# Kernel tuning notes

Measured on AMD Instinct MI355X. Metric: run time of the kernel, lower is better.

Reference implementation:

```python
import jax, jax.numpy as jnp
import numpy as np

N_NODES = 100000
IN_CH = 128
HID = 128
OUT_CH = 40
K = 3
N_EDGES = 3200000


def setup_inputs() -> dict:
    key = jax.random.key(0)
    ks = jax.random.split(key, 10)
    x = jax.random.normal(ks[0], (N_NODES, IN_CH), dtype=jnp.float32)
    edge_index = jax.random.randint(ks[1], (2, N_EDGES), 0, N_NODES, dtype=jnp.int64)
    s1 = 1.0 / np.sqrt(IN_CH)
    lin1_w = jax.random.uniform(ks[2], (IN_CH, HID), minval=-s1, maxval=s1, dtype=jnp.float32)
    lin1_b = jax.random.uniform(ks[3], (HID,), minval=-s1, maxval=s1, dtype=jnp.float32)
    s2 = 1.0 / np.sqrt(HID)
    gcn_w = jax.random.uniform(ks[4], (K, HID, HID), minval=-s2, maxval=s2, dtype=jnp.float32)
    gcn_b = jnp.zeros((K, HID), dtype=jnp.float32)
    lin2_w = jax.random.uniform(ks[5], (HID, OUT_CH), minval=-s2, maxval=s2, dtype=jnp.float32)
    lin2_b = jax.random.uniform(ks[6], (OUT_CH,), minval=-s2, maxval=s2, dtype=jnp.float32)
    return {"x": x, "edge_index": edge_index, "lin1_w": lin1_w, "lin1_b": lin1_b,
            "gcn_w": gcn_w, "gcn_b": gcn_b, "lin2_w": lin2_w, "lin2_b": lin2_b}


def _gcn_conv(h, w, b, src, dst, norm, n):
    # PyG GCNConv: transform, then symmetric-normalized aggregation (self-loops
    # already included in src/dst/norm), then bias.
    h = h @ w  # [N, H]
    msg = h[src] * norm[:, None]  # [E+N, H] gathered edge messages
    out = jax.ops.segment_sum(msg, dst, num_segments=n)
    return out + b


def reference(x, edge_index, lin1_w, lin1_b, gcn_w, gcn_b, lin2_w, lin2_b):
    n = x.shape[0]
    src, dst = edge_index[0], edge_index[1]
    # add self-loops (GCNConv default add_self_loops=True)
    loop = jnp.arange(n, dtype=src.dtype)
    src = jnp.concatenate([src, loop])
    dst = jnp.concatenate([dst, loop])
    # symmetric normalization D^{-1/2} (A+I) D^{-1/2}
    deg = jax.ops.segment_sum(jnp.ones(src.shape[0], dtype=x.dtype), dst, num_segments=n)
    dinv = jnp.where(deg > 0, jax.lax.rsqrt(deg), 0.0)
    norm = dinv[src] * dinv[dst]  # [E+N]

    h = jax.nn.relu(x @ lin1_w + lin1_b)  # dropout: eval mode (identity)
    for k in range(K):
        h = jax.nn.relu(_gcn_conv(h, gcn_w[k], gcn_b[k], src, dst, norm, n))
    logits = h @ lin2_w + lin2_b
    return jax.nn.log_softmax(logits, axis=1)
```

## Files before the change

kernel.cpp:

```cpp
#include <hip/hip_runtime.h>
#include <math.h>

#define NN 100000
#define NP 100032
#define HIDC 128
#define OUTC 40
#define NBUCK ((NN + 511) >> 9)
#define PT_TILE 8192
#define BCAP 18368
#define NRG 8
#define RG_SHIFT 14

typedef __attribute__((ext_vector_type(2))) float floatx2;
typedef __attribute__((ext_vector_type(4))) float floatx4;
typedef __attribute__((ext_vector_type(8))) short short8;
typedef __attribute__((ext_vector_type(4))) unsigned uintx4;

__device__ __forceinline__ unsigned pack_bf16x2(float a, float b) {
  unsigned ua = __float_as_uint(a), ub = __float_as_uint(b);
  ua = ua + 0x7fff + ((ua >> 16) & 1);
  ub = ub + 0x7fff + ((ub >> 16) & 1);
  return (ua >> 16) | (ub & 0xffff0000u);
}
__device__ __forceinline__ unsigned short bf16r(float x) {
  unsigned u = __float_as_uint(x);
  u = u + 0x7fff + ((u >> 16) & 1);
  return (unsigned short)(u >> 16);
}


__global__ __launch_bounds__(512) void partition_kernel(
    const int* __restrict__ src, const int* __restrict__ dst,
    int* __restrict__ bcur, unsigned* __restrict__ pairs, int E) {
  __shared__ int hist[256];
  __shared__ int lcur[256];
  __shared__ int startl[256];
  __shared__ int gofs[256];
  __shared__ unsigned lbuf[PT_TILE];
  int t = threadIdx.x;
  if (t < 256) { hist[t] = 0; lcur[t] = 0; }
  __syncthreads();
  int e0 = blockIdx.x * PT_TILE;
  int ec = E - e0; if (ec > PT_TILE) ec = PT_TILE;

  int dr[16], sr[16];
#pragma unroll
  for (int k = 0; k < 16; k++) {
    int i = t + (k << 9);
    if (i < ec) {
      int d = dst[e0 + i];
      dr[k] = d; sr[k] = src[e0 + i];
      atomicAdd(&hist[d >> 9], 1);
    }
  }
  __syncthreads();

  int h = (t < 256) ? hist[t] : 0;
  if (t < 256) startl[t] = h;
  __syncthreads();
  for (int off = 1; off < 256; off <<= 1) {
    int u = (t < 256 && t >= off) ? startl[t - off] : 0;
    __syncthreads();
    if (t < 256) startl[t] += u;
    __syncthreads();
  }
  if (t < 256) {
    int st = startl[t] - h;
    int gb = (h > 0) ? atomicAdd(&bcur[t], h) : 0;
    gofs[t] = gb - st;
    startl[t] = st;
  }
  __syncthreads();

#pragma unroll
  for (int k = 0; k < 16; k++) {
    int i = t + (k << 9);
    if (i < ec) {
      int d = dr[k];
      int b = d >> 9;
      int q = atomicAdd(&lcur[b], 1);
      lbuf[startl[b] + q] = ((unsigned)(d & 511) << 17) | (unsigned)sr[k];
    }
  }
  __syncthreads();

  for (int pos = t; pos < ec; pos += 512) {
    int lo = 0, hi = 255;
    while (lo < hi) {
      int mid = (lo + hi + 1) >> 1;
      if (startl[mid] <= pos) lo = mid; else hi = mid - 1;
    }
    pairs[gofs[lo] + pos] = lbuf[pos];
  }
}

__global__ __launch_bounds__(1024) void bucket_fill_kernel(
    const unsigned* __restrict__ pairs, const int* __restrict__ bcur,
    float* __restrict__ dinv, int* __restrict__ csr,
    int* __restrict__ sbeg, int* __restrict__ send,
    float* __restrict__ sdinv, int* __restrict__ sdn, int N) {
  int b = blockIdx.x;
  int d0 = b << 9;
  int nd = N - d0; if (nd > 512) nd = 512;
  __shared__ unsigned lbuf[BCAP];
  __shared__ unsigned short perm[BCAP];
  __shared__ int hist8[512 * NRG];
  __shared__ int cur8[512 * NRG];
  __shared__ int sums[512];
  __shared__ int dh[256];
  int t = threadIdx.x;
#pragma unroll
  for (int k = 0; k < NRG / 2; k++) hist8[t + k * 1024] = 0;
  int rbeg = b * BCAP;
  int cnt = bcur[b] - rbeg;
  for (int i = t; i < cnt; i += 1024) lbuf[i] = pairs[rbeg + i];
  __syncthreads();
  for (int i = t; i < cnt; i += 1024) {
    unsigned pk = lbuf[i];
    atomicAdd(&hist8[(int)(pk >> 17) * NRG + (int)((pk & 0x1FFFF) >> RG_SHIFT)], 1);
  }
  __syncthreads();
  int h = 0;
  int hr[NRG];
  if (t < 512) {
#pragma unroll
    for (int r = 0; r < NRG; r++) { hr[r] = hist8[t * NRG + r]; h += hr[r]; }
    sums[t] = h;
  }
  __syncthreads();
  for (int off = 1; off < 512; off <<= 1) {
    int u = (t < 512 && t >= off) ? sums[t - off] : 0;
    __syncthreads();
    if (t < 512) sums[t] += u;
    __syncthreads();
  }
  int lbase = 0; float di = 0.f;
  if (t < 512) {
    lbase = sums[t] - h;
    di = rsqrtf((float)(h + 1));
    int a = lbase;
#pragma unroll
    for (int r = 0; r < NRG; r++) { cur8[t * NRG + r] = a; a += hr[r]; }
    if (t < nd) dinv[d0 + t] = di;
  }
  __syncthreads();

  if (t < 128) dh[t] = 0;
  __syncthreads();
  int c = h < 127 ? h : 127;
  if (t < nd) atomicAdd(&dh[c], 1);
  __syncthreads();
  int dv = (t < 128) ? dh[t] : 0;
  if (t < 128) sums[t] = dv;
  __syncthreads();
  for (int off = 1; off < 128; off <<= 1) {
    int u = (t < 128 && t >= off) ? sums[t - off] : 0;
    __syncthreads();
    if (t < 128) sums[t] += u;
    __syncthreads();
  }
  if (t < 128) dh[128 + t] = sums[t] - dv;
  __syncthreads();
  if (t < nd) {
    int pos = d0 + atomicAdd(&dh[128 + c], 1);
    sbeg[pos] = rbeg + lbase; send[pos] = rbeg + lbase + h;
    sdinv[pos] = di; sdn[pos] = d0 + t;
  }
  __syncthreads();

  for (int i = t; i < cnt; i += 1024) {
    unsigned pk = lbuf[i];
    int q = atomicAdd(&cur8[(int)(pk >> 17) * NRG + (int)((pk & 0x1FFFF) >> RG_SHIFT)], 1);
    perm[q] = (unsigned short)i;
  }
  __syncthreads();

  for (int pos = t; pos < cnt; pos += 1024)
    csr[rbeg + pos] = (int)(lbuf[perm[pos]] & 0x1FFFF);
}


__global__ __launch_bounds__(256) void prep_misc_kernel(
    const float* __restrict__ lin1_w, const float* __restrict__ gcn_w,
    const float* __restrict__ lin2_w, int* __restrict__ bcur,
    unsigned short* __restrict__ Wt, unsigned short* __restrict__ W2t) {
  int b = blockIdx.x;
  int t = threadIdx.x;
  if (b == 0) {
    if (t < NBUCK) bcur[t] = t * BCAP;
  } else if (b <= 32) {
    int m = (b - 1) >> 3;
    int chunk = (b - 1) & 7;
    const float* src = (m == 0) ? lin1_w : (gcn_w + (size_t)(m - 1) * 16384);
    unsigned short* dstp = Wt + (size_t)m * 16384;
    int i0 = chunk * 2048;
    for (int i = i0 + t; i < i0 + 2048; i += 256) {
      int n = i >> 7, k = i & 127;
      dstp[(size_t)n * 128 + k] = bf16r(src[(size_t)k * 128 + n]);
    }
  } else {
    int chunk = b - 33;
    int i0 = chunk * 3072;
    for (int i = i0 + t; i < i0 + 3072; i += 256) {
      int n = i >> 7, k = i & 127;
      W2t[i] = (n < OUTC) ? bf16r(lin2_w[(size_t)k * OUTC + n]) : (unsigned short)0;
    }
  }
}


template <int MODE>
__global__ __launch_bounds__(256) void gemm_mfma_kernel(
    const void* __restrict__ Av, const unsigned short* __restrict__ Wt,
    const float* __restrict__ bias, const float* __restrict__ dinv,
    void* __restrict__ Y, int M) {
  int t = threadIdx.x;
  int w = t >> 6;
  int l = t & 63;
  int quad = l >> 4;
  int m16 = l & 15;
  int row0 = blockIdx.x * 64;
  int colbase = w * 32;

  floatx4 acc[4][2];
#pragma unroll
  for (int rt = 0; rt < 4; rt++)
#pragma unroll
    for (int ct = 0; ct < 2; ct++) acc[rt][ct] = (floatx4)0.f;

#pragma unroll
  for (int kc = 0; kc < 4; kc++) {
    int kof = kc * 32 + quad * 8;
    short8 a0 = *(const short8*)(Wt + (size_t)(colbase + m16) * 128 + kof);
    short8 a1 = *(const short8*)(Wt + (size_t)(colbase + 16 + m16) * 128 + kof);
#pragma unroll
    for (int rt = 0; rt < 4; rt++) {
      short8 bfr;
      if (MODE == 2) {
        const float* Af = (const float*)Av + (size_t)(row0 + rt * 16 + m16) * 128 + kof;
        float4 f0 = *(const float4*)Af;
        float4 f1 = *(const float4*)(Af + 4);
        unsigned u0 = pack_bf16x2(f0.x, f0.y);
        unsigned u1 = pack_bf16x2(f0.z, f0.w);
        unsigned u2 = pack_bf16x2(f1.x, f1.y);
        unsigned u3 = pack_bf16x2(f1.z, f1.w);
        bfr[0] = (short)(u0 & 0xFFFF); bfr[1] = (short)(u0 >> 16);
        bfr[2] = (short)(u1 & 0xFFFF); bfr[3] = (short)(u1 >> 16);
        bfr[4] = (short)(u2 & 0xFFFF); bfr[5] = (short)(u2 >> 16);
        bfr[6] = (short)(u3 & 0xFFFF); bfr[7] = (short)(u3 >> 16);
      } else {
        bfr = *(const short8*)((const unsigned short*)Av +
                               (size_t)(row0 + rt * 16 + m16) * 128 + kof);
      }
      acc[rt][0] = __builtin_amdgcn_mfma_f32_16x16x32_bf16(a0, bfr, acc[rt][0], 0, 0, 0);
      acc[rt][1] = __builtin_amdgcn_mfma_f32_16x16x32_bf16(a1, bfr, acc[rt][1], 0, 0, 0);
    }
  }

  if (MODE != 1) {
    unsigned short* Y16 = (unsigned short*)Y;
    float4 bv0 = *(const float4*)(bias + colbase + quad * 4);
    float4 bv1 = *(const float4*)(bias + colbase + 16 + quad * 4);
#pragma unroll
    for (int rt = 0; rt < 4; rt++) {
      int row = row0 + rt * 16 + m16;
      if (row < M) {
        uint2 s0, s1;
        s0.x = pack_bf16x2(fmaxf(acc[rt][0][0] + bv0.x, 0.f),
                           fmaxf(acc[rt][0][1] + bv0.y, 0.f));
        s0.y = pack_bf16x2(fmaxf(acc[rt][0][2] + bv0.z, 0.f),
                           fmaxf(acc[rt][0][3] + bv0.w, 0.f));
        s1.x = pack_bf16x2(fmaxf(acc[rt][1][0] + bv1.x, 0.f),
                           fmaxf(acc[rt][1][1] + bv1.y, 0.f));
        s1.y = pack_bf16x2(fmaxf(acc[rt][1][2] + bv1.z, 0.f),
                           fmaxf(acc[rt][1][3] + bv1.w, 0.f));
        *(uint2*)(Y16 + (size_t)row * 128 + colbase + quad * 4) = s0;
        *(uint2*)(Y16 + (size_t)row * 128 + colbase + 16 + quad * 4) = s1;
      }
    }
  } else {
    unsigned* Y8 = (unsigned*)Y;
#pragma unroll
    for (int rt = 0; rt < 4; rt++) {
      int row = row0 + rt * 16 + m16;
      if (row < M) {
        float dd = dinv[row];
        unsigned u0 = 0, u1 = 0;
        u0 = __builtin_amdgcn_cvt_pk_fp8_f32(acc[rt][0][0] * dd, acc[rt][0][1] * dd, (int)u0, false);
        u0 = __builtin_amdgcn_cvt_pk_fp8_f32(acc[rt][0][2] * dd, acc[rt][0][3] * dd, (int)u0, true);
        u1 = __builtin_amdgcn_cvt_pk_fp8_f32(acc[rt][1][0] * dd, acc[rt][1][1] * dd, (int)u1, false);
        u1 = __builtin_amdgcn_cvt_pk_fp8_f32(acc[rt][1][2] * dd, acc[rt][1][3] * dd, (int)u1, true);
        Y8[(size_t)row * 32 + (colbase >> 2) + quad] = u0;
        Y8[(size_t)row * 32 + ((colbase + 16) >> 2) + quad] = u1;
      }
    }
  }
}


#define ACC8(u)                                                       \
  acc[0] += __builtin_amdgcn_cvt_pk_f32_fp8((int)(u).x, false);       \
  acc[1] += __builtin_amdgcn_cvt_pk_f32_fp8((int)(u).x, true);        \
  acc[2] += __builtin_amdgcn_cvt_pk_f32_fp8((int)(u).y, false);       \
  acc[3] += __builtin_amdgcn_cvt_pk_f32_fp8((int)(u).y, true);        \
  acc[4] += __builtin_amdgcn_cvt_pk_f32_fp8((int)(u).z, false);       \
  acc[5] += __builtin_amdgcn_cvt_pk_f32_fp8((int)(u).z, true);        \
  acc[6] += __builtin_amdgcn_cvt_pk_f32_fp8((int)(u).w, false);       \
  acc[7] += __builtin_amdgcn_cvt_pk_f32_fp8((int)(u).w, true);

__global__ __launch_bounds__(256) void aggregate_fp8_kernel(
    const uint4* __restrict__ Ht8, const int* __restrict__ csr,
    const int* __restrict__ sbeg, const int* __restrict__ send,
    const float* __restrict__ sdinv, const int* __restrict__ sdn,
    const float* __restrict__ bias, uint4* __restrict__ Out, int N) {
  int wid = (blockIdx.x * blockDim.x + threadIdx.x) >> 6;
  int lane = threadIdx.x & 63;
  int g = lane >> 3;
  int c8 = lane & 7;
  int bucket = wid % NBUCK;
  int band = wid / NBUCK;
  int idx = (bucket << 9) + (band << 3) + g;
  if (idx >= N) return;
  int beg = sbeg[idx], end = send[idx];
  int d = sdn[idx];

  floatx2 acc[8];
  {
    uint4 us = Ht8[(size_t)d * 8 + c8];
    acc[0] = __builtin_amdgcn_cvt_pk_f32_fp8((int)us.x, false);
    acc[1] = __builtin_amdgcn_cvt_pk_f32_fp8((int)us.x, true);
    acc[2] = __builtin_amdgcn_cvt_pk_f32_fp8((int)us.y, false);
    acc[3] = __builtin_amdgcn_cvt_pk_f32_fp8((int)us.y, true);
    acc[4] = __builtin_amdgcn_cvt_pk_f32_fp8((int)us.z, false);
    acc[5] = __builtin_amdgcn_cvt_pk_f32_fp8((int)us.z, true);
    acc[6] = __builtin_amdgcn_cvt_pk_f32_fp8((int)us.w, false);
    acc[7] = __builtin_amdgcn_cvt_pk_f32_fp8((int)us.w, true);
  }
  int i = beg;
  int s0, s1, s2, s3, s4, s5, s6, s7;
  if (i + 7 < end) {
    s0 = csr[i];     s1 = csr[i + 1]; s2 = csr[i + 2]; s3 = csr[i + 3];
    s4 = csr[i + 4]; s5 = csr[i + 5]; s6 = csr[i + 6]; s7 = csr[i + 7];
  }
  while (i + 7 < end) {
    uint4 u0 = Ht8[(size_t)s0 * 8 + c8];
    uint4 u1 = Ht8[(size_t)s1 * 8 + c8];
    uint4 u2 = Ht8[(size_t)s2 * 8 + c8];
    uint4 u3 = Ht8[(size_t)s3 * 8 + c8];
    uint4 u4 = Ht8[(size_t)s4 * 8 + c8];
    uint4 u5 = Ht8[(size_t)s5 * 8 + c8];
    uint4 u6 = Ht8[(size_t)s6 * 8 + c8];
    uint4 u7 = Ht8[(size_t)s7 * 8 + c8];
    i += 8;
    if (i + 7 < end) {
      s0 = csr[i];     s1 = csr[i + 1]; s2 = csr[i + 2]; s3 = csr[i + 3];
      s4 = csr[i + 4]; s5 = csr[i + 5]; s6 = csr[i + 6]; s7 = csr[i + 7];
    }
    ACC8(u0) ACC8(u1) ACC8(u2) ACC8(u3) ACC8(u4) ACC8(u5) ACC8(u6) ACC8(u7)
  }
  if (i + 3 < end) {
    int t0 = csr[i], t1 = csr[i + 1], t2 = csr[i + 2], t3 = csr[i + 3];
    uint4 u0 = Ht8[(size_t)t0 * 8 + c8];
    uint4 u1 = Ht8[(size_t)t1 * 8 + c8];
    uint4 u2 = Ht8[(size_t)t2 * 8 + c8];
    uint4 u3 = Ht8[(size_t)t3 * 8 + c8];
    ACC8(u0) ACC8(u1) ACC8(u2) ACC8(u3)
    i += 4;
  }
  for (; i < end; ++i) {
    uint4 u0 = Ht8[(size_t)csr[i] * 8 + c8];
    ACC8(u0)
  }

  float dd = sdinv[idx];
  const float4* b4 = (const float4*)bias;
  float4 bv0 = b4[4 * c8 + 0];
  float4 bv1 = b4[4 * c8 + 1];
  float4 bv2 = b4[4 * c8 + 2];
  float4 bv3 = b4[4 * c8 + 3];
  uintx4 o0, o1;
  o0.x = pack_bf16x2(fmaxf(fmaf(dd, acc[0][0], bv0.x), 0.f),
                     fmaxf(fmaf(dd, acc[0][1], bv0.y), 0.f));
  o0.y = pack_bf16x2(fmaxf(fmaf(dd, acc[1][0], bv0.z), 0.f),
                     fmaxf(fmaf(dd, acc[1][1], bv0.w), 0.f));
  o0.z = pack_bf16x2(fmaxf(fmaf(dd, acc[2][0], bv1.x), 0.f),
                     fmaxf(fmaf(dd, acc[2][1], bv1.y), 0.f));
  o0.w = pack_bf16x2(fmaxf(fmaf(dd, acc[3][0], bv1.z), 0.f),
                     fmaxf(fmaf(dd, acc[3][1], bv1.w), 0.f));
  o1.x = pack_bf16x2(fmaxf(fmaf(dd, acc[4][0], bv2.x), 0.f),
                     fmaxf(fmaf(dd, acc[4][1], bv2.y), 0.f));
  o1.y = pack_bf16x2(fmaxf(fmaf(dd, acc[5][0], bv2.z), 0.f),
                     fmaxf(fmaf(dd, acc[5][1], bv2.w), 0.f));
  o1.z = pack_bf16x2(fmaxf(fmaf(dd, acc[6][0], bv3.x), 0.f),
                     fmaxf(fmaf(dd, acc[6][1], bv3.y), 0.f));
  o1.w = pack_bf16x2(fmaxf(fmaf(dd, acc[7][0], bv3.z), 0.f),
                     fmaxf(fmaf(dd, acc[7][1], bv3.w), 0.f));
  __builtin_nontemporal_store(o0, (uintx4*)(Out + (size_t)d * 16 + 2 * c8));
  __builtin_nontemporal_store(o1, (uintx4*)(Out + (size_t)d * 16 + 2 * c8 + 1));
}


__global__ __launch_bounds__(256) void head_mfma_kernel(
    const unsigned short* __restrict__ A, const unsigned short* __restrict__ W2t,
    const float* __restrict__ b2, float* __restrict__ Out, int N) {
  __shared__ float lg[64][48];
  __shared__ float bs[48];
  int t = threadIdx.x;
  int w = t >> 6, l = t & 63, quad = l >> 4, m16 = l & 15;
  if (t < 48) bs[t] = (t < OUTC) ? b2[t] : 0.f;
  int row0 = blockIdx.x * 64;

  floatx4 acc[3];
  acc[0] = (floatx4)0.f; acc[1] = (floatx4)0.f; acc[2] = (floatx4)0.f;
  const unsigned short* Aw = A + (size_t)(row0 + w * 16) * 128;
#pragma unroll
  for (int kc = 0; kc < 4; kc++) {
    int kof = kc * 32 + quad * 8;
    short8 a = *(const short8*)(Aw + (size_t)m16 * 128 + kof);
#pragma unroll
    for (int ct = 0; ct < 3; ct++) {
      short8 b = *(const short8*)(W2t + (size_t)(ct * 16 + m16) * 128 + kof);
      acc[ct] = __builtin_amdgcn_mfma_f32_16x16x32_bf16(a, b, acc[ct], 0, 0, 0);
    }
  }
#pragma unroll
  for (int ct = 0; ct < 3; ct++)
#pragma unroll
    for (int j = 0; j < 4; j++)
      lg[w * 16 + quad * 4 + j][ct * 16 + m16] = acc[ct][j];
  __syncthreads();

  int r = t >> 2, sub = t & 3;
  int row = row0 + r;
  float vals[10];
  float mx = -3.4e38f;
#pragma unroll
  for (int j = 0; j < 10; j++) {
    float v = lg[r][sub * 10 + j] + bs[sub * 10 + j];
    vals[j] = v;
    mx = fmaxf(mx, v);
  }
  mx = fmaxf(mx, __shfl_xor(mx, 1, 64));
  mx = fmaxf(mx, __shfl_xor(mx, 2, 64));
  float se = 0.f;
#pragma unroll
  for (int j = 0; j < 10; j++) se += expf(vals[j] - mx);
  se += __shfl_xor(se, 1, 64);
  se += __shfl_xor(se, 2, 64);
  if (row < N) {
    float ls = logf(se);
#pragma unroll
    for (int j = 0; j < 10; j++)
      Out[(size_t)row * OUTC + sub * 10 + j] = vals[j] - mx - ls;
  }
}


extern "C" void kernel_launch(void* const* d_in, const int* in_sizes, int n_in,
                              void* d_out, int out_size, void* d_ws, size_t ws_size,
                              hipStream_t stream) {
  const float* x      = (const float*)d_in[0];
  const int*   edge   = (const int*)d_in[1];
  const float* lin1_w = (const float*)d_in[2];
  const float* lin1_b = (const float*)d_in[3];
  const float* gcn_w  = (const float*)d_in[4];
  const float* gcn_b  = (const float*)d_in[5];
  const float* lin2_w = (const float*)d_in[6];
  const float* lin2_b = (const float*)d_in[7];
  float* out = (float*)d_out;

  const int N = NN;
  const int E = in_sizes[1] / 2;
  const int* src = edge;
  const int* dst = edge + E;

  char* p = (char*)d_ws;
  auto alloc = [&](size_t bytes) { char* q = p; p += (bytes + 255) & ~(size_t)255; return q; };
  unsigned*       hA16    = (unsigned*)alloc((size_t)NP * 128 * 2);
  unsigned*       hB8     = (unsigned*)alloc((size_t)NP * 32 * 4);
  unsigned*       pairs   = (unsigned*)alloc((size_t)NBUCK * BCAP * 4);
  int*            csr     = (int*)alloc((size_t)NBUCK * BCAP * 4);
  float*          dinv    = (float*)alloc((size_t)NP * 4);
  int*            sbeg    = (int*)alloc((size_t)N * 4);
  int*            send    = (int*)alloc((size_t)N * 4);
  float*          sdinv   = (float*)alloc((size_t)N * 4);
  int*            sdn     = (int*)alloc((size_t)N * 4);
  unsigned short* Wt      = (unsigned short*)alloc((size_t)4 * 16384 * 2);
  unsigned short* W2t     = (unsigned short*)alloc((size_t)48 * 128 * 2);
  int*            bcur    = (int*)alloc(256 * 4);

  prep_misc_kernel<<<35, 256, 0, stream>>>(lin1_w, gcn_w, lin2_w, bcur, Wt, W2t);
  partition_kernel<<<(E + PT_TILE - 1) / PT_TILE, 512, 0, stream>>>(src, dst, bcur, pairs, E);
  bucket_fill_kernel<<<NBUCK, 1024, 0, stream>>>(pairs, bcur, dinv, csr,
                                                 sbeg, send, sdinv, sdn, N);

  int gb = NP / 64;
  gemm_mfma_kernel<2><<<gb, 256, 0, stream>>>((const void*)x, Wt,
                                              lin1_b, nullptr, (void*)hA16, N);
  int ablocks = (NBUCK * 64) / 4;
  for (int k = 0; k < 3; k++) {
    gemm_mfma_kernel<1><<<gb, 256, 0, stream>>>((const void*)hA16,
                                                Wt + (size_t)(k + 1) * 16384,
                                                nullptr, dinv, (void*)hB8, N);
    aggregate_fp8_kernel<<<ablocks, 256, 0, stream>>>(
        (const uint4*)hB8, csr, sbeg, send, sdinv, sdn, gcn_b + (size_t)k * 128,
        (uint4*)hA16, N);
  }
  head_mfma_kernel<<<gb, 256, 0, stream>>>((const unsigned short*)hA16, W2t,
                                           lin2_b, out, N);
}
```

Before: 454.8 us.

## Interleave two destination nodes per wave and walk neighbors by source-range groups

The aggregation kernel now has each 8-lane group process two destination nodes, paired from opposite ends of the degree-sorted slot order to balance work. Each node's neighbor list is walked in eight segments split by source-node range, interleaving the two nodes so that concurrent waves gather from similar regions of the feature table and get better cache locality. Bucket fill now writes eight per-range start offsets per node, which adds metadata traffic. The deeper 8-wide gather prefetch is replaced by a simpler 4-wide loop per segment, which may reduce memory-level parallelism.

```diff
diff --git a/kernel.cpp b/kernel.cpp
--- a/kernel.cpp
+++ b/kernel.cpp
@@ -10,6 +10,7 @@
 #define BCAP 18368
 #define NRG 8
 #define RG_SHIFT 14
+#define NSLOT (NBUCK * 64)
 
 typedef __attribute__((ext_vector_type(2))) float floatx2;
 typedef __attribute__((ext_vector_type(4))) float floatx4;
@@ -97,7 +98,7 @@
 __global__ __launch_bounds__(1024) void bucket_fill_kernel(
     const unsigned* __restrict__ pairs, const int* __restrict__ bcur,
     float* __restrict__ dinv, int* __restrict__ csr,
-    int* __restrict__ sbeg, int* __restrict__ send,
+    int* __restrict__ sbeg8, int* __restrict__ send,
     float* __restrict__ sdinv, int* __restrict__ sdn, int N) {
   int b = blockIdx.x;
   int d0 = b << 9;
@@ -163,8 +164,11 @@
   __syncthreads();
   if (t < nd) {
     int pos = d0 + atomicAdd(&dh[128 + c], 1);
-    sbeg[pos] = rbeg + lbase; send[pos] = rbeg + lbase + h;
+    send[pos] = rbeg + lbase + h;
     sdinv[pos] = di; sdn[pos] = d0 + t;
+    int a = rbeg + lbase;
+#pragma unroll
+    for (int r = 0; r < NRG; r++) { sbeg8[(size_t)pos * NRG + r] = a; a += hr[r]; }
   }
   __syncthreads();
 
@@ -298,105 +302,118 @@
 }
 
 
-#define ACC8(u)                                                       \
-  acc[0] += __builtin_amdgcn_cvt_pk_f32_fp8((int)(u).x, false);       \
-  acc[1] += __builtin_amdgcn_cvt_pk_f32_fp8((int)(u).x, true);        \
-  acc[2] += __builtin_amdgcn_cvt_pk_f32_fp8((int)(u).y, false);       \
-  acc[3] += __builtin_amdgcn_cvt_pk_f32_fp8((int)(u).y, true);        \
-  acc[4] += __builtin_amdgcn_cvt_pk_f32_fp8((int)(u).z, false);       \
-  acc[5] += __builtin_amdgcn_cvt_pk_f32_fp8((int)(u).z, true);        \
-  acc[6] += __builtin_amdgcn_cvt_pk_f32_fp8((int)(u).w, false);       \
-  acc[7] += __builtin_amdgcn_cvt_pk_f32_fp8((int)(u).w, true);
+#define ACC8V(a, u)                                                     \
+  a[0] += __builtin_amdgcn_cvt_pk_f32_fp8((int)(u).x, false);           \
+  a[1] += __builtin_amdgcn_cvt_pk_f32_fp8((int)(u).x, true);            \
+  a[2] += __builtin_amdgcn_cvt_pk_f32_fp8((int)(u).y, false);           \
+  a[3] += __builtin_amdgcn_cvt_pk_f32_fp8((int)(u).y, true);            \
+  a[4] += __builtin_amdgcn_cvt_pk_f32_fp8((int)(u).z, false);           \
+  a[5] += __builtin_amdgcn_cvt_pk_f32_fp8((int)(u).z, true);            \
+  a[6] += __builtin_amdgcn_cvt_pk_f32_fp8((int)(u).w, false);           \
+  a[7] += __builtin_amdgcn_cvt_pk_f32_fp8((int)(u).w, true);
+
+#define INIT8(a, d)                                                     \
+  {                                                                     \
+    uint4 us = Ht8[(size_t)(d) * 8 + c8];                               \
+    a[0] = __builtin_amdgcn_cvt_pk_f32_fp8((int)us.x, false);           \
+    a[1] = __builtin_amdgcn_cvt_pk_f32_fp8((int)us.x, true);            \
+    a[2] = __builtin_amdgcn_cvt_pk_f32_fp8((int)us.y, false);           \
+    a[3] = __builtin_amdgcn_cvt_pk_f32_fp8((int)us.y, true);            \
+    a[4] = __builtin_amdgcn_cvt_pk_f32_fp8((int)us.z, false);           \
+    a[5] = __builtin_amdgcn_cvt_pk_f32_fp8((int)us.z, true);            \
+    a[6] = __builtin_amdgcn_cvt_pk_f32_fp8((int)us.w, false);           \
+    a[7] = __builtin_amdgcn_cvt_pk_f32_fp8((int)us.w, true);            \
+  }
+
+#define SEG(a, b, e)                                                    \
+  {                                                                     \
+    int i = b;                                                          \
+    while (i + 3 < e) {                                                 \
+      int t0 = csr[i], t1 = csr[i + 1], t2 = csr[i + 2], t3 = csr[i + 3]; \
+      uint4 u0 = Ht8[(size_t)t0 * 8 + c8];                              \
+      uint4 u1 = Ht8[(size_t)t1 * 8 + c8];                              \
+      uint4 u2 = Ht8[(size_t)t2 * 8 + c8];                              \
+      uint4 u3 = Ht8[(size_t)t3 * 8 + c8];                              \
+      i += 4;                                                           \
+      ACC8V(a, u0) ACC8V(a, u1) ACC8V(a, u2) ACC8V(a, u3)               \
+    }                                                                   \
+    for (; i < e; ++i) {                                                \
+      uint4 u0 = Ht8[(size_t)csr[i] * 8 + c8];                          \
+      ACC8V(a, u0)                                                      \
+    }                                                                   \
+  }
+
+#define EPILOGUE(a, idx, d)                                             \
+  {                                                                     \
+    float dd = sdinv[idx];                                              \
+    uintx4 o0, o1;                                                      \
+    o0.x = pack_bf16x2(fmaxf(fmaf(dd, a[0][0], bv0.x), 0.f),            \
+                       fmaxf(fmaf(dd, a[0][1], bv0.y), 0.f));           \
+    o0.y = pack_bf16x2(fmaxf(fmaf(dd, a[1][0], bv0.z), 0.f),            \
+                       fmaxf(fmaf(dd, a[1][1], bv0.w), 0.f));           \
+    o0.z = pack_bf16x2(fmaxf(fmaf(dd, a[2][0], bv1.x), 0.f),            \
+                       fmaxf(fmaf(dd, a[2][1], bv1.y), 0.f));           \
+    o0.w = pack_bf16x2(fmaxf(fmaf(dd, a[3][0], bv1.z), 0.f),            \
+                       fmaxf(fmaf(dd, a[3][1], bv1.w), 0.f));           \
+    o1.x = pack_bf16x2(fmaxf(fmaf(dd, a[4][0], bv2.x), 0.f),            \
+                       fmaxf(fmaf(dd, a[4][1], bv2.y), 0.f));           \
+    o1.y = pack_bf16x2(fmaxf(fmaf(dd, a[5][0], bv2.z), 0.f),            \
+                       fmaxf(fmaf(dd, a[5][1], bv2.w), 0.f));           \
+    o1.z = pack_bf16x2(fmaxf(fmaf(dd, a[6][0], bv3.x), 0.f),            \
+                       fmaxf(fmaf(dd, a[6][1], bv3.y), 0.f));           \
+    o1.w = pack_bf16x2(fmaxf(fmaf(dd, a[7][0], bv3.z), 0.f),            \
+                       fmaxf(fmaf(dd, a[7][1], bv3.w), 0.f));           \
+    __builtin_nontemporal_store(o0, (uintx4*)(Out + (size_t)(d) * 16 + 2 * c8));     \
+    __builtin_nontemporal_store(o1, (uintx4*)(Out + (size_t)(d) * 16 + 2 * c8 + 1)); \
+  }
 
 __global__ __launch_bounds__(256) void aggregate_fp8_kernel(
     const uint4* __restrict__ Ht8, const int* __restrict__ csr,
-    const int* __restrict__ sbeg, const int* __restrict__ send,
+    const int* __restrict__ sbeg8, const int* __restrict__ send,
     const float* __restrict__ sdinv, const int* __restrict__ sdn,
     const float* __restrict__ bias, uint4* __restrict__ Out, int N) {
   int wid = (blockIdx.x * blockDim.x + threadIdx.x) >> 6;
   int lane = threadIdx.x & 63;
   int g = lane >> 3;
   int c8 = lane & 7;
-  int bucket = wid % NBUCK;
-  int band = wid / NBUCK;
-  int idx = (bucket << 9) + (band << 3) + g;
-  if (idx >= N) return;
-  int beg = sbeg[idx], end = send[idx];
-  int d = sdn[idx];
-
-  floatx2 acc[8];
-  {
-    uint4 us = Ht8[(size_t)d * 8 + c8];
-    acc[0] = __builtin_amdgcn_cvt_pk_f32_fp8((int)us.x, false);
-    acc[1] = __builtin_amdgcn_cvt_pk_f32_fp8((int)us.x, true);
-    acc[2] = __builtin_amdgcn_cvt_pk_f32_fp8((int)us.y, false);
-    acc[3] = __builtin_amdgcn_cvt_pk_f32_fp8((int)us.y, true);
-    acc[4] = __builtin_amdgcn_cvt_pk_f32_fp8((int)us.z, false);
-    acc[5] = __builtin_amdgcn_cvt_pk_f32_fp8((int)us.z, true);
-    acc[6] = __builtin_amdgcn_cvt_pk_f32_fp8((int)us.w, false);
-    acc[7] = __builtin_amdgcn_cvt_pk_f32_fp8((int)us.w, true);
-  }
-  int i = beg;
-  int s0, s1, s2, s3, s4, s5, s6, s7;
-  if (i + 7 < end) {
-    s0 = csr[i];     s1 = csr[i + 1]; s2 = csr[i + 2]; s3 = csr[i + 3];
-    s4 = csr[i + 4]; s5 = csr[i + 5]; s6 = csr[i + 6]; s7 = csr[i + 7];
-  }
-  while (i + 7 < end) {
-    uint4 u0 = Ht8[(size_t)s0 * 8 + c8];
-    uint4 u1 = Ht8[(size_t)s1 * 8 + c8];
-    uint4 u2 = Ht8[(size_t)s2 * 8 + c8];
-    uint4 u3 = Ht8[(size_t)s3 * 8 + c8];
-    uint4 u4 = Ht8[(size_t)s4 * 8 + c8];
-    uint4 u5 = Ht8[(size_t)s5 * 8 + c8];
-    uint4 u6 = Ht8[(size_t)s6 * 8 + c8];
-    uint4 u7 = Ht8[(size_t)s7 * 8 + c8];
-    i += 8;
-    if (i + 7 < end) {
-      s0 = csr[i];     s1 = csr[i + 1]; s2 = csr[i + 2]; s3 = csr[i + 3];
-      s4 = csr[i + 4]; s5 = csr[i + 5]; s6 = csr[i + 6]; s7 = csr[i + 7];
-    }
-    ACC8(u0) ACC8(u1) ACC8(u2) ACC8(u3) ACC8(u4) ACC8(u5) ACC8(u6) ACC8(u7)
-  }
-  if (i + 3 < end) {
-    int t0 = csr[i], t1 = csr[i + 1], t2 = csr[i + 2], t3 = csr[i + 3];
-    uint4 u0 = Ht8[(size_t)t0 * 8 + c8];
-    uint4 u1 = Ht8[(size_t)t1 * 8 + c8];
-    uint4 u2 = Ht8[(size_t)t2 * 8 + c8];
-    uint4 u3 = Ht8[(size_t)t3 * 8 + c8];
-    ACC8(u0) ACC8(u1) ACC8(u2) ACC8(u3)
-    i += 4;
-  }
-  for (; i < end; ++i) {
-    uint4 u0 = Ht8[(size_t)csr[i] * 8 + c8];
-    ACC8(u0)
-  }
-
-  float dd = sdinv[idx];
+
+  int sA = wid;
+  int sB = NSLOT - 1 - wid;
+  int bkA = sA % NBUCK, bdA = sA / NBUCK;
+  int bkB = sB % NBUCK, bdB = sB / NBUCK;
+  int idxA = (bkA << 9) + (bdA << 3) + g;
+  int idxB = (bkB << 9) + (bdB << 3) + g;
+  bool vA = idxA < N, vB = idxB < N;
+
+  int dA = 0, dB = 0, endA = 0, endB = 0;
+  if (vA) { dA = sdn[idxA]; endA = send[idxA]; }
+  if (vB) { dB = sdn[idxB]; endB = send[idxB]; }
+
+  floatx2 aA[8], aB[8];
+  if (vA) INIT8(aA, dA);
+  if (vB) INIT8(aB, dB);
+
+#pragma unroll
+  for (int r = 0; r < NRG; r++) {
+    if (vA) {
+      int b = sbeg8[(size_t)idxA * NRG + r];
+      int e = (r < NRG - 1) ? sbeg8[(size_t)idxA * NRG + r + 1] : endA;
+      SEG(aA, b, e)
+    }
+    if (vB) {
+      int b = sbeg8[(size_t)idxB * NRG + r];
+      int e = (r < NRG - 1) ? sbeg8[(size_t)idxB * NRG + r + 1] : endB;
+      SEG(aB, b, e)
+    }
+  }
+
   const float4* b4 = (const float4*)bias;
   float4 bv0 = b4[4 * c8 + 0];
   float4 bv1 = b4[4 * c8 + 1];
   float4 bv2 = b4[4 * c8 + 2];
   float4 bv3 = b4[4 * c8 + 3];
-  uintx4 o0, o1;
-  o0.x = pack_bf16x2(fmaxf(fmaf(dd, acc[0][0], bv0.x), 0.f),
-                     fmaxf(fmaf(dd, acc[0][1], bv0.y), 0.f));
-  o0.y = pack_bf16x2(fmaxf(fmaf(dd, acc[1][0], bv0.z), 0.f),
-                     fmaxf(fmaf(dd, acc[1][1], bv0.w), 0.f));
-  o0.z = pack_bf16x2(fmaxf(fmaf(dd, acc[2][0], bv1.x), 0.f),
-                     fmaxf(fmaf(dd, acc[2][1], bv1.y), 0.f));
-  o0.w = pack_bf16x2(fmaxf(fmaf(dd, acc[3][0], bv1.z), 0.f),
-                     fmaxf(fmaf(dd, acc[3][1], bv1.w), 0.f));
-  o1.x = pack_bf16x2(fmaxf(fmaf(dd, acc[4][0], bv2.x), 0.f),
-                     fmaxf(fmaf(dd, acc[4][1], bv2.y), 0.f));
-  o1.y = pack_bf16x2(fmaxf(fmaf(dd, acc[5][0], bv2.z), 0.f),
-                     fmaxf(fmaf(dd, acc[5][1], bv2.w), 0.f));
-  o1.z = pack_bf16x2(fmaxf(fmaf(dd, acc[6][0], bv3.x), 0.f),
-                     fmaxf(fmaf(dd, acc[6][1], bv3.y), 0.f));
-  o1.w = pack_bf16x2(fmaxf(fmaf(dd, acc[7][0], bv3.z), 0.f),
-                     fmaxf(fmaf(dd, acc[7][1], bv3.w), 0.f));
-  __builtin_nontemporal_store(o0, (uintx4*)(Out + (size_t)d * 16 + 2 * c8));
-  __builtin_nontemporal_store(o1, (uintx4*)(Out + (size_t)d * 16 + 2 * c8 + 1));
+  if (vA) EPILOGUE(aA, idxA, dA)
+  if (vB) EPILOGUE(aB, idxB, dB)
 }
 
 
@@ -481,10 +498,10 @@
   unsigned*       pairs   = (unsigned*)alloc((size_t)NBUCK * BCAP * 4);
   int*            csr     = (int*)alloc((size_t)NBUCK * BCAP * 4);
   float*          dinv    = (float*)alloc((size_t)NP * 4);
-  int*            sbeg    = (int*)alloc((size_t)N * 4);
-  int*            send    = (int*)alloc((size_t)N * 4);
-  float*          sdinv   = (float*)alloc((size_t)N * 4);
-  int*            sdn     = (int*)alloc((size_t)N * 4);
+  int*            sbeg8   = (int*)alloc((size_t)NN * NRG * 4);
+  int*            send    = (int*)alloc((size_t)NN * 4);
+  float*          sdinv   = (float*)alloc((size_t)NN * 4);
+  int*            sdn     = (int*)alloc((size_t)NN * 4);
   unsigned short* Wt      = (unsigned short*)alloc((size_t)4 * 16384 * 2);
   unsigned short* W2t     = (unsigned short*)alloc((size_t)48 * 128 * 2);
   int*            bcur    = (int*)alloc(256 * 4);
@@ -492,18 +509,18 @@
   prep_misc_kernel<<<35, 256, 0, stream>>>(lin1_w, gcn_w, lin2_w, bcur, Wt, W2t);
   partition_kernel<<<(E + PT_TILE - 1) / PT_TILE, 512, 0, stream>>>(src, dst, bcur, pairs, E);
   bucket_fill_kernel<<<NBUCK, 1024, 0, stream>>>(pairs, bcur, dinv, csr,
-                                                 sbeg, send, sdinv, sdn, N);
+                                                 sbeg8, send, sdinv, sdn, N);
 
   int gb = NP / 64;
   gemm_mfma_kernel<2><<<gb, 256, 0, stream>>>((const void*)x, Wt,
                                               lin1_b, nullptr, (void*)hA16, N);
-  int ablocks = (NBUCK * 64) / 4;
+  int ablocks = (NSLOT / 2 + 3) / 4;
   for (int k = 0; k < 3; k++) {
     gemm_mfma_kernel<1><<<gb, 256, 0, stream>>>((const void*)hA16,
                                                 Wt + (size_t)(k + 1) * 16384,
                                                 nullptr, dinv, (void*)hB8, N);
     aggregate_fp8_kernel<<<ablocks, 256, 0, stream>>>(
-        (const uint4*)hB8, csr, sbeg, send, sdinv, sdn, gcn_b + (size_t)k * 128,
+        (const uint4*)hB8, csr, sbeg8, send, sdinv, sdn, gcn_b + (size_t)k * 128,
         (uint4*)hA16, N);
   }
   head_mfma_kernel<<<gb, 256, 0, stream>>>((const unsigned short*)hA16, W2t,
```

Result: slower. 599.7 us (+31.9%).
